# Kernel optimization log

Measured on AMD Instinct MI355X. Metric: run time of the kernel, lower is better.

## Reference

```python
import jax, jax.numpy as jnp
import numpy as np

N_X, N_Y, D = 8192, 512, None  # D set below
D = 512

def setup_inputs() -> dict:
    key = jax.random.key(0)
    kx, ky = jax.random.split(key)
    x = jax.random.normal(kx, (8192, D), dtype=jnp.float32)
    y = jax.random.normal(ky, (8192, D), dtype=jnp.float32)
    gamma = jnp.float32(1.0)  # learnable scalar parameter, init value from __init__
    return {"x": x, "y": y, "gamma": gamma}

def reference(x, y, gamma):
    # K_{ij} = exp(-gamma * ||x_i - y_j||^2)
    x2 = jnp.sum(x * x, axis=1)[:, None]          # [n_x, 1]
    y2 = jnp.sum(y * y, axis=1)[None, :]          # [1, n_y]
    xy = x @ y.T                                  # [n_x, n_y] GEMM
    sq = jnp.maximum(x2 + y2 - 2.0 * xy, 0.0)     # clamp tiny negatives from cancellation
    return jnp.exp(-gamma * sq)
```

## Files before the change

### kernel.cpp

```cpp
#include <hip/hip_runtime.h>
#include <hip/hip_bf16.h>

typedef unsigned char u8;
typedef unsigned short u16;
typedef unsigned int u32;
typedef int i32x8 __attribute__((ext_vector_type(8)));
typedef float f32x4 __attribute__((ext_vector_type(4)));

#define NX 8192
#define NY 8192
#define D  512
#define BM 128
#define BN 128
#define BK 128

#define SCALE_ONE 0x7F7F7F7F

__device__ __forceinline__ void async16(void* lds, const void* g) {
    __builtin_amdgcn_global_load_lds(
        (const __attribute__((address_space(1))) void*)g,
        (__attribute__((address_space(3))) void*)lds,
        16, 0, 0);
}

__global__ __launch_bounds__(256) void prep_kernel(
    const float* __restrict__ x, const float* __restrict__ y,
    u8* __restrict__ xq, u8* __restrict__ yq,
    float* __restrict__ x2, float* __restrict__ y2)
{
    const int lane = threadIdx.x & 63;
    const int row  = blockIdx.x * 4 + (threadIdx.x >> 6);
    const float* src; u8* dst; float* nrm;
    if (row < NX) {
        src = x + (size_t)row * D; dst = xq + (size_t)row * D; nrm = x2 + row;
    } else {
        const int r = row - NX;
        src = y + (size_t)r * D; dst = yq + (size_t)r * D; nrm = y2 + r;
    }
    float4 v0 = *(const float4*)(src + lane * 8);
    float4 v1 = *(const float4*)(src + lane * 8 + 4);
    float s = v0.x*v0.x + v0.y*v0.y + v0.z*v0.z + v0.w*v0.w
            + v1.x*v1.x + v1.y*v1.y + v1.z*v1.z + v1.w*v1.w;
    u32 p0 = 0, p1 = 0;
    p0 = __builtin_amdgcn_cvt_pk_fp8_f32(v0.x, v0.y, p0, false);
    p0 = __builtin_amdgcn_cvt_pk_fp8_f32(v0.z, v0.w, p0, true);
    p1 = __builtin_amdgcn_cvt_pk_fp8_f32(v1.x, v1.y, p1, false);
    p1 = __builtin_amdgcn_cvt_pk_fp8_f32(v1.z, v1.w, p1, true);
    uint2 pk = make_uint2(p0, p1);
    *(uint2*)(dst + lane * 8) = pk;

    #pragma unroll
    for (int o = 32; o > 0; o >>= 1) s += __shfl_down(s, o);
    if (lane == 0) *nrm = s;
}

__global__ __launch_bounds__(256) void rbf_kernel(
    const u8* __restrict__ xq, const u8* __restrict__ yq,
    const float* __restrict__ x2, const float* __restrict__ y2,
    const float* __restrict__ gamma_p, float* __restrict__ out)
{
    __shared__ u8 As[2][BM * BK];
    __shared__ u8 Bs[2][BN * BK];

    const int t    = threadIdx.x;
    const int lane = t & 63;
    const int wid  = t >> 6;
    const int wr   = wid >> 1;
    const int wc   = wid & 1;

    const int nwg = gridDim.x;
    const int cpx = nwg >> 3;
    const int bid = blockIdx.x;
    const int swz = (bid & 7) * cpx + (bid >> 3);
    const int brow = swz >> 6;
    const int bcol = swz & 63;

    const size_t row0 = (size_t)brow * BM;
    const size_t col0 = (size_t)bcol * BN;

    const int c0 = wid * 4;
    const int lr = lane >> 3;
    const int lc = (lane & 7) * 16;

    auto stage = [&](int buf, int kt) {
        #pragma unroll
        for (int i = 0; i < 4; ++i) {
            const int c = c0 + i;
            async16(&As[buf][c * 1024], xq + (row0 + (size_t)(c * 8 + lr)) * D + kt + lc);
        }
        #pragma unroll
        for (int i = 0; i < 4; ++i) {
            const int c = c0 + i;
            async16(&Bs[buf][c * 1024], yq + (col0 + (size_t)(c * 8 + lr)) * D + kt + lc);
        }
    };

    stage(0, 0);
    __syncthreads();

    f32x4 acc[4][4] = {};
    const int ko = (lane >> 4) * 32;
    const int ar = (lane & 15);

    #pragma unroll
    for (int kt = 0; kt < 4; ++kt) {
        if (kt < 3) stage((kt + 1) & 1, (kt + 1) * BK);
        const int cur = kt & 1;
        i32x8 a[4], b[4];
        #pragma unroll
        for (int m = 0; m < 4; ++m)
            a[m] = *(const i32x8*)&As[cur][(wr * 64 + m * 16 + ar) * BK + ko];
        #pragma unroll
        for (int n = 0; n < 4; ++n)
            b[n] = *(const i32x8*)&Bs[cur][(wc * 64 + n * 16 + ar) * BK + ko];
        #pragma unroll
        for (int m = 0; m < 4; ++m)
            #pragma unroll
            for (int n = 0; n < 4; ++n)
                acc[m][n] = __builtin_amdgcn_mfma_scale_f32_16x16x128_f8f6f4(
                    a[m], b[n], acc[m][n],
                    0 , 0 ,
                    0, SCALE_ONE, 0, SCALE_ONE);
        if (kt < 3) __syncthreads();
    }

    const float gamma = *gamma_p;
    const int rl = (lane >> 4) * 4;
    const int cl = lane & 15;
    #pragma unroll
    for (int m = 0; m < 4; ++m) {
        #pragma unroll
        for (int j = 0; j < 4; ++j) {
            const size_t gr = row0 + wr * 64 + m * 16 + rl + j;
            const float xn = x2[gr];
            float* orow = out + gr * (size_t)NY + col0 + wc * 64 + cl;
            #pragma unroll
            for (int n = 0; n < 4; ++n) {
                const float yn = y2[col0 + wc * 64 + n * 16 + cl];
                float sq = xn + yn - 2.0f * acc[m][n][j];
                sq = fmaxf(sq, 0.0f);
                __builtin_nontemporal_store(__expf(-gamma * sq), &orow[n * 16]);
            }
        }
    }
}

extern "C" void kernel_launch(void* const* d_in, const int* in_sizes, int n_in,
                              void* d_out, int out_size, void* d_ws, size_t ws_size,
                              hipStream_t stream) {
    const float* x = (const float*)d_in[0];
    const float* y = (const float*)d_in[1];
    const float* gamma_p = (const float*)d_in[2];
    float* out = (float*)d_out;

    u8* xq = (u8*)d_ws;
    u8* yq = xq + (size_t)NX * D;
    float* x2 = (float*)(yq + (size_t)NY * D);
    float* y2 = x2 + NX;

    prep_kernel<<<(NX + NY) / 4, 256, 0, stream>>>(x, y, xq, yq, x2, y2);

    const int grid = (NX / BM) * (NY / BN);
    rbf_kernel<<<grid, 256, 0, stream>>>(xq, yq, x2, y2, gamma_p, out);
}
```

Measured before the change: 317.6 us.

## Halve K tile, swizzle LDS layout, use fp8 16x16x32 MFMA with higher occupancy

```diff
diff --git a/kernel.cpp b/kernel.cpp
--- a/kernel.cpp
+++ b/kernel.cpp
@@ -4,7 +4,6 @@
 typedef unsigned char u8;
 typedef unsigned short u16;
 typedef unsigned int u32;
-typedef int i32x8 __attribute__((ext_vector_type(8)));
 typedef float f32x4 __attribute__((ext_vector_type(4)));
 
 #define NX 8192
@@ -12,9 +11,7 @@
 #define D  512
 #define BM 128
 #define BN 128
-#define BK 128
-
-#define SCALE_ONE 0x7F7F7F7F
+#define BK 64
 
 __device__ __forceinline__ void async16(void* lds, const void* g) {
     __builtin_amdgcn_global_load_lds(
@@ -54,7 +51,7 @@
     if (lane == 0) *nrm = s;
 }
 
-__global__ __launch_bounds__(256) void rbf_kernel(
+__global__ __launch_bounds__(256, 4) void rbf_kernel(
     const u8* __restrict__ xq, const u8* __restrict__ yq,
     const float* __restrict__ x2, const float* __restrict__ y2,
     const float* __restrict__ gamma_p, float* __restrict__ out)
@@ -78,20 +75,21 @@
     const size_t row0 = (size_t)brow * BM;
     const size_t col0 = (size_t)bcol * BN;
 
-    const int c0 = wid * 4;
-    const int lr = lane >> 3;
-    const int lc = (lane & 7) * 16;
+    const int crow = lane >> 2;
+    const int scol = (((lane & 3) ^ ((lane >> 3) & 3)) << 4);
 
     auto stage = [&](int buf, int kt) {
         #pragma unroll
-        for (int i = 0; i < 4; ++i) {
-            const int c = c0 + i;
-            async16(&As[buf][c * 1024], xq + (row0 + (size_t)(c * 8 + lr)) * D + kt + lc);
+        for (int i = 0; i < 2; ++i) {
+            const int c = wid * 2 + i;
+            async16(&As[buf][c * 1024],
+                    xq + (row0 + (size_t)(c * 16 + crow)) * D + kt + scol);
         }
         #pragma unroll
-        for (int i = 0; i < 4; ++i) {
-            const int c = c0 + i;
-            async16(&Bs[buf][c * 1024], yq + (col0 + (size_t)(c * 8 + lr)) * D + kt + lc);
+        for (int i = 0; i < 2; ++i) {
+            const int c = wid * 2 + i;
+            async16(&Bs[buf][c * 1024],
+                    yq + (col0 + (size_t)(c * 16 + crow)) * D + kt + scol);
         }
     };
 
@@ -99,29 +97,34 @@
     __syncthreads();
 
     f32x4 acc[4][4] = {};
-    const int ko = (lane >> 4) * 32;
-    const int ar = (lane & 15);
+    const int ar = lane & 15;
+    const int kg = lane >> 4;
+    const int sw = (ar >> 1) & 3;
+    const int hb = (kg & 1) * 8;
+    const int ug = kg >> 1;
 
     #pragma unroll
-    for (int kt = 0; kt < 4; ++kt) {
-        if (kt < 3) stage((kt + 1) & 1, (kt + 1) * BK);
+    for (int kt = 0; kt < 8; ++kt) {
+        if (kt < 7) stage((kt + 1) & 1, (kt + 1) * BK);
         const int cur = kt & 1;
-        i32x8 a[4], b[4];
         #pragma unroll
-        for (int m = 0; m < 4; ++m)
-            a[m] = *(const i32x8*)&As[cur][(wr * 64 + m * 16 + ar) * BK + ko];
-        #pragma unroll
-        for (int n = 0; n < 4; ++n)
-            b[n] = *(const i32x8*)&Bs[cur][(wc * 64 + n * 16 + ar) * BK + ko];
-        #pragma unroll
-        for (int m = 0; m < 4; ++m)
+        for (int ks = 0; ks < 2; ++ks) {
+            const int po = (((ks * 2 + ug) ^ sw) << 4) + hb;
+            long a_[4], b_[4];
+            #pragma unroll
+            for (int m = 0; m < 4; ++m)
+                a_[m] = *(const long*)&As[cur][(wr * 64 + m * 16 + ar) * BK + po];
             #pragma unroll
             for (int n = 0; n < 4; ++n)
-                acc[m][n] = __builtin_amdgcn_mfma_scale_f32_16x16x128_f8f6f4(
-                    a[m], b[n], acc[m][n],
-                    0 , 0 ,
-                    0, SCALE_ONE, 0, SCALE_ONE);
-        if (kt < 3) __syncthreads();
+                b_[n] = *(const long*)&Bs[cur][(wc * 64 + n * 16 + ar) * BK + po];
+            #pragma unroll
+            for (int m = 0; m < 4; ++m)
+                #pragma unroll
+                for (int n = 0; n < 4; ++n)
+                    acc[m][n] = __builtin_amdgcn_mfma_f32_16x16x32_fp8_fp8(
+                        a_[m], b_[n], acc[m][n], 0, 0, 0);
+        }
+        if (kt < 7) __syncthreads();
     }
 
     const float gamma = *gamma_p;
```

After: 322.2 us. Within noise of the previous version (+1.4%).
